# Kernel tuning notes

Hardware: AMD Instinct MI355X
Metric: run time of the kernel (lower is better)

## Reference

```python
import jax, jax.numpy as jnp
import numpy as np

N = 50000   # nodes
E = 800000  # edges
D = 128     # input_dim
H = 128     # hidden_dim
C = 40      # output_dim (classes)


def setup_inputs() -> dict:
    key = jax.random.key(0)
    ks = jax.random.split(key, 8)
    x = jax.random.normal(ks[0], (N, D), dtype=jnp.float32)
    edge_index = jax.random.randint(ks[1], (2, E), 0, N, dtype=jnp.int32)
    sD = 1.0 / np.sqrt(D)
    sH = 1.0 / np.sqrt(H)
    W1 = jax.random.uniform(ks[2], (D, H), jnp.float32, -sD, sD)
    b1 = jnp.zeros((H,), jnp.float32)
    W2 = jax.random.uniform(ks[3], (H, H), jnp.float32, -sH, sH)
    b2 = jnp.zeros((H,), jnp.float32)
    W3 = jax.random.uniform(ks[4], (H, C), jnp.float32, -sH, sH)
    b3 = jnp.zeros((C,), jnp.float32)
    return {"x": x, "edge_index": edge_index,
            "W1": W1, "b1": b1, "W2": W2, "b2": b2, "W3": W3, "b3": b3}


def reference(x, edge_index, W1, b1, W2, b2, W3, b3):
    # GCNConv: out = D^{-1/2} (A + I) D^{-1/2} (x @ W) + b
    src = edge_index[0]
    dst = edge_index[1]
    loop = jnp.arange(N, dtype=src.dtype)
    src_f = jnp.concatenate([src, loop])  # [E+N] with self-loops
    dst_f = jnp.concatenate([dst, loop])
    deg = jax.ops.segment_sum(jnp.ones(E + N, x.dtype), dst_f, num_segments=N)
    dinv = jax.lax.rsqrt(jnp.maximum(deg, 1.0))  # deg >= 1 due to self-loops
    norm = dinv[src_f] * dinv[dst_f]  # [E+N]

    def conv(h, W, b):
        h = h @ W                       # [N, F_out]
        msg = h[src_f] * norm[:, None]  # [E+N, F_out] gathered messages
        return jax.ops.segment_sum(msg, dst_f, num_segments=N) + b

    h = jax.nn.relu(conv(x, W1, b1))
    h = jax.nn.relu(conv(h, W2, b2))  # dropout is identity in eval mode
    return conv(h, W3, b3)
```

## Files before the change

### kernel.cpp

```cpp
#include <hip/hip_runtime.h>

typedef unsigned short ushort_t;
typedef unsigned int uint_t;


__global__ void k_deg_count(const int* __restrict__ ei, int* __restrict__ deg, int E) {
    int e = blockIdx.x * blockDim.x + threadIdx.x;
    if (e < E) atomicAdd(&deg[ei[E + e]], 1);
}

__global__ void k_bsum(const int* __restrict__ deg, int* __restrict__ bsum, int n) {
    __shared__ int s[256];
    int t = threadIdx.x;
    int i = blockIdx.x * 256 + t;
    s[t] = (i < n) ? deg[i] : 0;
    __syncthreads();
    for (int off = 128; off > 0; off >>= 1) {
        if (t < off) s[t] += s[t + off];
        __syncthreads();
    }
    if (t == 0) bsum[blockIdx.x] = s[0];
}

__global__ void k_bscan(int* __restrict__ bsum, int* __restrict__ tot, int nb) {
    __shared__ int s[1024];
    int t = threadIdx.x;
    int v = (t < nb) ? bsum[t] : 0;
    s[t] = v;
    __syncthreads();
    for (int off = 1; off < 1024; off <<= 1) {
        int u = (t >= off) ? s[t - off] : 0;
        __syncthreads();
        s[t] += u;
        __syncthreads();
    }
    if (t < nb) bsum[t] = s[t] - v;
    if (t == nb - 1) tot[0] = s[t];
}

__global__ void k_rowptr(const int* __restrict__ deg, const int* __restrict__ bsum,
                         int* __restrict__ rowptr, int* __restrict__ cursor,
                         float* __restrict__ dinv, int n) {
    __shared__ int s[256];
    int t = threadIdx.x;
    int i = blockIdx.x * 256 + t;
    int v = (i < n) ? deg[i] : 0;
    s[t] = v;
    __syncthreads();
    for (int off = 1; off < 256; off <<= 1) {
        int u = (t >= off) ? s[t - off] : 0;
        __syncthreads();
        s[t] += u;
        __syncthreads();
    }
    if (i < n) {
        int ex = bsum[blockIdx.x] + s[t] - v;
        rowptr[i] = ex;
        cursor[i] = ex;
        dinv[i] = rsqrtf((float)(v + 1));
    }
}

__global__ __launch_bounds__(256) void k_fill(const int* __restrict__ ei,
                                              int* __restrict__ cursor,
                                              int* __restrict__ csr, int E, int n) {
    const int xcd = blockIdx.x & 7;
    const int e = (blockIdx.x >> 3) * 256 + threadIdx.x;
    if (e >= E) return;
    int d = ei[E + e];
    const int lo = (int)(((long long)xcd * n) >> 3);
    const int hi = (int)(((long long)(xcd + 1) * n) >> 3);
    if (d < lo || d >= hi) return;
    int s = ei[e];
    int pos = atomicAdd(&cursor[d], 1);
    csr[pos] = s;
}

__device__ __forceinline__ ushort_t f2bf_rne(float f) {
    uint_t u = __float_as_uint(f);
    u += 0x7fffu + ((u >> 16) & 1u);
    return (ushort_t)(u >> 16);
}
__device__ __forceinline__ float bflo(uint_t u) {
    return __uint_as_float(u << 16);
}
__device__ __forceinline__ float bfhi(uint_t u) {
    return __uint_as_float(u & 0xffff0000u);
}

__global__ __launch_bounds__(256) void k_gemm128(const float* __restrict__ X,
                                                 const float* __restrict__ W,
                                                 ushort_t* __restrict__ Y, int N) {
    __shared__ float sX[32][68];
    __shared__ float sW[32][128];
    const int tid = threadIdx.x;
    const int bm = blockIdx.x * 64;
    const int m0 = (tid >> 4) * 4;
    const int c4 = (tid & 15) * 4;
    const int xr = tid >> 3;
    const int xf = tid & 7;
    float acc[4][8] = {};
    for (int k0 = 0; k0 < 128; k0 += 32) {
        #pragma unroll
        for (int rr = 0; rr < 2; ++rr) {
            int row = bm + xr + rr * 32;
            int rc = min(row, N - 1);
            float4 v = *(const float4*)(X + (size_t)rc * 128 + k0 + xf * 4);
            int m = xr + rr * 32;
            sX[xf * 4 + 0][m] = v.x;
            sX[xf * 4 + 1][m] = v.y;
            sX[xf * 4 + 2][m] = v.z;
            sX[xf * 4 + 3][m] = v.w;
        }
        #pragma unroll
        for (int it = 0; it < 4; ++it) {
            int i = tid + it * 256;
            int wr = i >> 5;
            int wf = i & 31;
            *(float4*)(&sW[wr][wf * 4]) =
                *(const float4*)(W + (size_t)(k0 + wr) * 128 + wf * 4);
        }
        __syncthreads();
        #pragma unroll
        for (int kk = 0; kk < 32; ++kk) {
            float4 a  = *(const float4*)(&sX[kk][m0]);
            float4 b0 = *(const float4*)(&sW[kk][c4]);
            float4 b1 = *(const float4*)(&sW[kk][64 + c4]);
            float av[4] = {a.x, a.y, a.z, a.w};
            float bv[8] = {b0.x, b0.y, b0.z, b0.w, b1.x, b1.y, b1.z, b1.w};
            #pragma unroll
            for (int r = 0; r < 4; ++r)
                #pragma unroll
                for (int c = 0; c < 8; ++c)
                    acc[r][c] = fmaf(av[r], bv[c], acc[r][c]);
        }
        __syncthreads();
    }
    #pragma unroll
    for (int r = 0; r < 4; ++r) {
        int row = bm + m0 + r;
        if (row < N) {
            ushort4 o0 = {f2bf_rne(acc[r][0]), f2bf_rne(acc[r][1]),
                          f2bf_rne(acc[r][2]), f2bf_rne(acc[r][3])};
            ushort4 o1 = {f2bf_rne(acc[r][4]), f2bf_rne(acc[r][5]),
                          f2bf_rne(acc[r][6]), f2bf_rne(acc[r][7])};
            *(ushort4*)(Y + (size_t)row * 128 + c4)      = o0;
            *(ushort4*)(Y + (size_t)row * 128 + 64 + c4) = o1;
        }
    }
}

__global__ __launch_bounds__(256) void k_gemm40(const float* __restrict__ X,
                                                const float* __restrict__ W,
                                                ushort_t* __restrict__ Y, int N) {
    __shared__ float sX[32][132];
    __shared__ float sW[32][40];
    const int tid = threadIdx.x;
    const int bm = blockIdx.x * 128;
    const int m0 = (tid >> 3) * 4;
    const int n0 = (tid & 7) * 5;
    const int xf = tid & 7;
    float acc[4][5] = {};
    for (int k0 = 0; k0 < 128; k0 += 32) {
        #pragma unroll
        for (int it = 0; it < 4; ++it) {
            int i = tid + it * 256;
            int row = bm + (i >> 3);
            int rc = min(row, N - 1);
            float4 v = *(const float4*)(X + (size_t)rc * 128 + k0 + xf * 4);
            int m = i >> 3;
            sX[xf * 4 + 0][m] = v.x;
            sX[xf * 4 + 1][m] = v.y;
            sX[xf * 4 + 2][m] = v.z;
            sX[xf * 4 + 3][m] = v.w;
        }
        for (int i = tid; i < 320; i += 256) {
            int wr = i / 10;
            int wf = i - wr * 10;
            *(float4*)(&sW[wr][wf * 4]) =
                *(const float4*)(W + (size_t)(k0 + wr) * 40 + wf * 4);
        }
        __syncthreads();
        #pragma unroll
        for (int kk = 0; kk < 32; ++kk) {
            float4 a = *(const float4*)(&sX[kk][m0]);
            float av[4] = {a.x, a.y, a.z, a.w};
            #pragma unroll
            for (int c = 0; c < 5; ++c) {
                float b = sW[kk][n0 + c];
                #pragma unroll
                for (int r = 0; r < 4; ++r)
                    acc[r][c] = fmaf(av[r], b, acc[r][c]);
            }
        }
        __syncthreads();
    }
    #pragma unroll
    for (int r = 0; r < 4; ++r) {
        int row = bm + m0 + r;
        if (row < N) {
            #pragma unroll
            for (int c = 0; c < 5; ++c)
                Y[(size_t)row * 64 + n0 + c] = f2bf_rne(acc[r][c]);
        }
    }
}

template <bool RELU>
__global__ __launch_bounds__(256) void k_agg128(
        const ushort_t* __restrict__ XW, const int* __restrict__ rowptr,
        const int* __restrict__ csr, const float* __restrict__ dinv,
        const float* __restrict__ bias, float* __restrict__ out, int n) {
    const int lane = threadIdx.x & 31;
    const int sub  = threadIdx.x >> 5;
    const int g = blockIdx.x;
    const int xcd = g & 7;
    const int slice = xcd >> 2;
    const int pair = (g >> 3) * 4 + (xcd & 3);
    const int d = pair * 8 + sub;
    if (d >= n) return;
    const uint_t* xw = (const uint_t*)XW;
    const int fb = slice * 32 + lane;
    float dv = dinv[d];
    float w0 = dv * dv;
    uint_t sq = xw[(size_t)d * 64 + fb];
    float2 a;
    a.x = w0 * bflo(sq);
    a.y = w0 * bfhi(sq);
    int j = rowptr[d], end = rowptr[d + 1];
    for (; j + 8 <= end; j += 8) {
        int s0 = csr[j + 0], s1 = csr[j + 1], s2 = csr[j + 2], s3 = csr[j + 3];
        int s4 = csr[j + 4], s5 = csr[j + 5], s6 = csr[j + 6], s7 = csr[j + 7];
        float w0e = dinv[s0] * dv, w1e = dinv[s1] * dv;
        float w2e = dinv[s2] * dv, w3e = dinv[s3] * dv;
        float w4e = dinv[s4] * dv, w5e = dinv[s5] * dv;
        float w6e = dinv[s6] * dv, w7e = dinv[s7] * dv;
        uint_t u0 = xw[(size_t)s0 * 64 + fb];
        uint_t u1 = xw[(size_t)s1 * 64 + fb];
        uint_t u2 = xw[(size_t)s2 * 64 + fb];
        uint_t u3 = xw[(size_t)s3 * 64 + fb];
        uint_t u4 = xw[(size_t)s4 * 64 + fb];
        uint_t u5 = xw[(size_t)s5 * 64 + fb];
        uint_t u6 = xw[(size_t)s6 * 64 + fb];
        uint_t u7 = xw[(size_t)s7 * 64 + fb];
        a.x = fmaf(w0e, bflo(u0), a.x); a.y = fmaf(w0e, bfhi(u0), a.y);
        a.x = fmaf(w1e, bflo(u1), a.x); a.y = fmaf(w1e, bfhi(u1), a.y);
        a.x = fmaf(w2e, bflo(u2), a.x); a.y = fmaf(w2e, bfhi(u2), a.y);
        a.x = fmaf(w3e, bflo(u3), a.x); a.y = fmaf(w3e, bfhi(u3), a.y);
        a.x = fmaf(w4e, bflo(u4), a.x); a.y = fmaf(w4e, bfhi(u4), a.y);
        a.x = fmaf(w5e, bflo(u5), a.x); a.y = fmaf(w5e, bfhi(u5), a.y);
        a.x = fmaf(w6e, bflo(u6), a.x); a.y = fmaf(w6e, bfhi(u6), a.y);
        a.x = fmaf(w7e, bflo(u7), a.x); a.y = fmaf(w7e, bfhi(u7), a.y);
    }
    for (; j < end; ++j) {
        int s = csr[j];
        float we = dinv[s] * dv;
        uint_t u = xw[(size_t)s * 64 + fb];
        a.x = fmaf(we, bflo(u), a.x);
        a.y = fmaf(we, bfhi(u), a.y);
    }
    float2 b = ((const float2*)bias)[fb];
    a.x += b.x; a.y += b.y;
    if (RELU) {
        a.x = fmaxf(a.x, 0.f);
        a.y = fmaxf(a.y, 0.f);
    }
    ((float2*)out)[(size_t)d * 64 + fb] = a;
}

__global__ __launch_bounds__(256) void k_agg40(
        const ushort_t* __restrict__ XW, const int* __restrict__ rowptr,
        const int* __restrict__ csr, const float* __restrict__ dinv,
        const float* __restrict__ bias, float* __restrict__ out, int n) {
    const int lane = threadIdx.x & 31;
    const int sub  = threadIdx.x >> 5;
    const int d = blockIdx.x * 8 + sub;
    if (d >= n || lane >= 20) return;
    const uint_t* xw = (const uint_t*)XW;
    float dv = dinv[d];
    float w0 = dv * dv;
    uint_t sq = xw[(size_t)d * 32 + lane];
    float2 a;
    a.x = w0 * bflo(sq);
    a.y = w0 * bfhi(sq);
    int j = rowptr[d], end = rowptr[d + 1];
    for (; j + 4 <= end; j += 4) {
        int s0 = csr[j + 0], s1 = csr[j + 1], s2 = csr[j + 2], s3 = csr[j + 3];
        float w0e = dinv[s0] * dv, w1e = dinv[s1] * dv;
        float w2e = dinv[s2] * dv, w3e = dinv[s3] * dv;
        uint_t u0 = xw[(size_t)s0 * 32 + lane];
        uint_t u1 = xw[(size_t)s1 * 32 + lane];
        uint_t u2 = xw[(size_t)s2 * 32 + lane];
        uint_t u3 = xw[(size_t)s3 * 32 + lane];
        a.x = fmaf(w0e, bflo(u0), a.x); a.y = fmaf(w0e, bfhi(u0), a.y);
        a.x = fmaf(w1e, bflo(u1), a.x); a.y = fmaf(w1e, bfhi(u1), a.y);
        a.x = fmaf(w2e, bflo(u2), a.x); a.y = fmaf(w2e, bfhi(u2), a.y);
        a.x = fmaf(w3e, bflo(u3), a.x); a.y = fmaf(w3e, bfhi(u3), a.y);
    }
    for (; j < end; ++j) {
        int s = csr[j];
        float we = dinv[s] * dv;
        uint_t u = xw[(size_t)s * 32 + lane];
        a.x = fmaf(we, bflo(u), a.x);
        a.y = fmaf(we, bfhi(u), a.y);
    }
    float2 b = ((const float2*)bias)[lane];
    a.x += b.x; a.y += b.y;
    ((float2*)out)[(size_t)d * 20 + lane] = a;
}

static inline int cdiv(long long a, int b) { return (int)((a + b - 1) / b); }

extern "C" void kernel_launch(void* const* d_in, const int* in_sizes, int n_in,
                              void* d_out, int out_size, void* d_ws, size_t ws_size,
                              hipStream_t stream) {
    const float* x  = (const float*)d_in[0];
    const int*   ei = (const int*)d_in[1];
    const float* W1 = (const float*)d_in[2];
    const float* b1 = (const float*)d_in[3];
    const float* W2 = (const float*)d_in[4];
    const float* b2 = (const float*)d_in[5];
    const float* W3 = (const float*)d_in[6];
    const float* b3 = (const float*)d_in[7];
    float* out = (float*)d_out;

    const int N = in_sizes[0] / 128;
    const int E = in_sizes[1] / 2;

    char* ws = (char*)d_ws;
    int*   deg    = (int*)ws;                 ws += (size_t)N * 4;
    int*   rowptr = (int*)ws;                 ws += (size_t)(N + 1) * 4;
    int*   cursor = (int*)ws;                 ws += (size_t)N * 4;
    float* dinv   = (float*)ws;               ws += (size_t)N * 4;
    int*   bsum   = (int*)ws;                 ws += (size_t)1024 * 4;
    ws = (char*)(((uintptr_t)ws + 127) & ~(uintptr_t)127);
    int*   csr    = (int*)ws;                 ws += (size_t)E * 4;
    char*  bufA   = ws;                       ws += (size_t)N * 128 * 4;
    float* bufB   = (float*)ws;

    const int BT = 256;
    const int nb = cdiv(N, 256);
    const int ndg = cdiv(N, 8);
    const int agg128Grid = cdiv(ndg, 4) * 8;

    hipMemsetAsync(deg, 0, (size_t)N * 4, stream);
    k_deg_count<<<cdiv(E, BT), BT, 0, stream>>>(ei, deg, E);
    k_bsum<<<nb, 256, 0, stream>>>(deg, bsum, N);
    k_bscan<<<1, 1024, 0, stream>>>(bsum, rowptr + N, nb);
    k_rowptr<<<nb, 256, 0, stream>>>(deg, bsum, rowptr, cursor, dinv, N);
    k_fill<<<cdiv(E, BT) * 8, 256, 0, stream>>>(ei, cursor, csr, E, N);

    k_gemm128<<<cdiv(N, 64), 256, 0, stream>>>(x, W1, (ushort_t*)bufA, N);
    k_agg128<true><<<agg128Grid, 256, 0, stream>>>((const ushort_t*)bufA, rowptr, csr, dinv, b1, bufB, N);
    k_gemm128<<<cdiv(N, 64), 256, 0, stream>>>(bufB, W2, (ushort_t*)bufA, N);
    k_agg128<true><<<agg128Grid, 256, 0, stream>>>((const ushort_t*)bufA, rowptr, csr, dinv, b2, bufB, N);
    k_gemm40<<<cdiv(N, 128), 256, 0, stream>>>(bufB, W3, (ushort_t*)bufA, N);
    k_agg40<<<cdiv(N, 8), 256, 0, stream>>>((const ushort_t*)bufA, rowptr, csr, dinv, b3, out, N);
}
```

Measured before the change: 342.5 us.

## Use one full wave per node in 128-wide aggregation, drop XCD feature slicing

The 128-feature aggregation kernel now assigns one 64-lane wave to each destination node and covers all features, instead of half-waves covering feature halves with blocks spread so each XCD owns one feature slice. This removes the duplicated neighbor-index and degree loads and gathers each neighbor row as one contiguous access. In exchange it gives up the per-XCD L2 locality that came from each XCD touching only half the feature table.

```diff
diff --git a/kernel.cpp b/kernel.cpp
--- a/kernel.cpp
+++ b/kernel.cpp
@@ -211,19 +211,14 @@
         const ushort_t* __restrict__ XW, const int* __restrict__ rowptr,
         const int* __restrict__ csr, const float* __restrict__ dinv,
         const float* __restrict__ bias, float* __restrict__ out, int n) {
-    const int lane = threadIdx.x & 31;
-    const int sub  = threadIdx.x >> 5;
-    const int g = blockIdx.x;
-    const int xcd = g & 7;
-    const int slice = xcd >> 2;
-    const int pair = (g >> 3) * 4 + (xcd & 3);
-    const int d = pair * 8 + sub;
+    const int lane = threadIdx.x & 63;
+    const int wv = __builtin_amdgcn_readfirstlane(threadIdx.x >> 6);
+    const int d = blockIdx.x * 4 + wv;
     if (d >= n) return;
     const uint_t* xw = (const uint_t*)XW;
-    const int fb = slice * 32 + lane;
     float dv = dinv[d];
     float w0 = dv * dv;
-    uint_t sq = xw[(size_t)d * 64 + fb];
+    uint_t sq = xw[(size_t)d * 64 + lane];
     float2 a;
     a.x = w0 * bflo(sq);
     a.y = w0 * bfhi(sq);
@@ -235,14 +230,14 @@
         float w2e = dinv[s2] * dv, w3e = dinv[s3] * dv;
         float w4e = dinv[s4] * dv, w5e = dinv[s5] * dv;
         float w6e = dinv[s6] * dv, w7e = dinv[s7] * dv;
-        uint_t u0 = xw[(size_t)s0 * 64 + fb];
-        uint_t u1 = xw[(size_t)s1 * 64 + fb];
-        uint_t u2 = xw[(size_t)s2 * 64 + fb];
-        uint_t u3 = xw[(size_t)s3 * 64 + fb];
-        uint_t u4 = xw[(size_t)s4 * 64 + fb];
-        uint_t u5 = xw[(size_t)s5 * 64 + fb];
-        uint_t u6 = xw[(size_t)s6 * 64 + fb];
-        uint_t u7 = xw[(size_t)s7 * 64 + fb];
+        uint_t u0 = xw[(size_t)s0 * 64 + lane];
+        uint_t u1 = xw[(size_t)s1 * 64 + lane];
+        uint_t u2 = xw[(size_t)s2 * 64 + lane];
+        uint_t u3 = xw[(size_t)s3 * 64 + lane];
+        uint_t u4 = xw[(size_t)s4 * 64 + lane];
+        uint_t u5 = xw[(size_t)s5 * 64 + lane];
+        uint_t u6 = xw[(size_t)s6 * 64 + lane];
+        uint_t u7 = xw[(size_t)s7 * 64 + lane];
         a.x = fmaf(w0e, bflo(u0), a.x); a.y = fmaf(w0e, bfhi(u0), a.y);
         a.x = fmaf(w1e, bflo(u1), a.x); a.y = fmaf(w1e, bfhi(u1), a.y);
         a.x = fmaf(w2e, bflo(u2), a.x); a.y = fmaf(w2e, bfhi(u2), a.y);
@@ -255,17 +250,17 @@
     for (; j < end; ++j) {
         int s = csr[j];
         float we = dinv[s] * dv;
-        uint_t u = xw[(size_t)s * 64 + fb];
+        uint_t u = xw[(size_t)s * 64 + lane];
         a.x = fmaf(we, bflo(u), a.x);
         a.y = fmaf(we, bfhi(u), a.y);
     }
-    float2 b = ((const float2*)bias)[fb];
+    float2 b = ((const float2*)bias)[lane];
     a.x += b.x; a.y += b.y;
     if (RELU) {
         a.x = fmaxf(a.x, 0.f);
         a.y = fmaxf(a.y, 0.f);
     }
-    ((float2*)out)[(size_t)d * 64 + fb] = a;
+    ((float2*)out)[(size_t)d * 64 + lane] = a;
 }
 
 __global__ __launch_bounds__(256) void k_agg40(
@@ -340,8 +335,6 @@
 
     const int BT = 256;
     const int nb = cdiv(N, 256);
-    const int ndg = cdiv(N, 8);
-    const int agg128Grid = cdiv(ndg, 4) * 8;
 
     hipMemsetAsync(deg, 0, (size_t)N * 4, stream);
     k_deg_count<<<cdiv(E, BT), BT, 0, stream>>>(ei, deg, E);
@@ -351,9 +344,9 @@
     k_fill<<<cdiv(E, BT) * 8, 256, 0, stream>>>(ei, cursor, csr, E, N);
 
     k_gemm128<<<cdiv(N, 64), 256, 0, stream>>>(x, W1, (ushort_t*)bufA, N);
-    k_agg128<true><<<agg128Grid, 256, 0, stream>>>((const ushort_t*)bufA, rowptr, csr, dinv, b1, bufB, N);
+    k_agg128<true><<<cdiv(N, 4), 256, 0, stream>>>((const ushort_t*)bufA, rowptr, csr, dinv, b1, bufB, N);
     k_gemm128<<<cdiv(N, 64), 256, 0, stream>>>(bufB, W2, (ushort_t*)bufA, N);
-    k_agg128<true><<<agg128Grid, 256, 0, stream>>>((const ushort_t*)bufA, rowptr, csr, dinv, b2, bufB, N);
+    k_agg128<true><<<cdiv(N, 4), 256, 0, stream>>>((const ushort_t*)bufA, rowptr, csr, dinv, b2, bufB, N);
     k_gemm40<<<cdiv(N, 128), 256, 0, stream>>>(bufB, W3, (ushort_t*)bufA, N);
     k_agg40<<<cdiv(N, 8), 256, 0, stream>>>((const ushort_t*)bufA, rowptr, csr, dinv, b3, out, N);
 }
```

After: 327.5 us. 1.05x faster.
